# Performance work log

Measured on AMD Instinct MI355X. Metric: run time of the kernel, lower is better.

Reference implementation:

```python
import jax, jax.numpy as jnp
import numpy as np
from jax import lax

EPS = 1e-5

def _conv3x3(x, w, stride=1):
    # x: [B,C,H,W], w: [O,I,3,3]
    dn = lax.conv_dimension_numbers(x.shape, w.shape, ('NCHW', 'OIHW', 'NCHW'))
    return lax.conv_general_dilated(x, w, window_strides=(stride, stride),
                                    padding=((1, 1), (1, 1)), dimension_numbers=dn)

def _batchnorm(x, gamma, beta):
    # training-mode BN over (N,H,W) per channel
    mean = jnp.mean(x, axis=(0, 2, 3), keepdims=True)
    var = jnp.var(x, axis=(0, 2, 3), keepdims=True)
    inv = lax.rsqrt(var + EPS)
    return (x - mean) * inv * gamma[None, :, None, None] + beta[None, :, None, None]

def setup_inputs() -> dict:
    key = jax.random.key(0)
    ks = jax.random.split(key, 8)
    B, C, H, W, E = 16, 256, 64, 64, 512
    x = jax.random.normal(ks[0], (B, C, H, W), dtype=jnp.float32)
    embedding = jax.random.normal(ks[1], (B, E), dtype=jnp.float32)
    s_conv = 1.0 / np.sqrt(C * 9)
    conv1_w = jax.random.normal(ks[2], (C, C, 3, 3), dtype=jnp.float32) * s_conv
    conv2_w = jax.random.normal(ks[3], (C, C, 3, 3), dtype=jnp.float32) * s_conv
    s_g = 1.0 / np.sqrt(E)
    g1_w = jax.random.normal(ks[4], (E, C), dtype=jnp.float32) * s_g
    g1_b = jnp.zeros((C,), dtype=jnp.float32)
    g2_w = jax.random.normal(ks[5], (E, C), dtype=jnp.float32) * s_g
    g2_b = jnp.zeros((C,), dtype=jnp.float32)
    bn1_g = jnp.ones((C,), dtype=jnp.float32)
    bn1_b = jnp.zeros((C,), dtype=jnp.float32)
    bn2_g = jnp.ones((C,), dtype=jnp.float32)
    bn2_b = jnp.zeros((C,), dtype=jnp.float32)
    return {"x": x, "embedding": embedding, "conv1_w": conv1_w, "conv2_w": conv2_w,
            "g1_w": g1_w, "g1_b": g1_b, "g2_w": g2_w, "g2_b": g2_b,
            "bn1_g": bn1_g, "bn1_b": bn1_b, "bn2_g": bn2_g, "bn2_b": bn2_b}

def reference(x, embedding, conv1_w, conv2_w, g1_w, g1_b, g2_w, g2_b,
              bn1_g, bn1_b, bn2_g, bn2_b):
    identity = x
    # gate 1: per-sample per-channel gate values (softmax over channels)
    gate1 = jax.nn.softmax(embedding @ g1_w + g1_b, axis=-1)  # [B,C]
    out = _conv3x3(x, conv1_w, stride=1) * gate1[:, :, None, None]
    out = jax.nn.relu(_batchnorm(out, bn1_g, bn1_b))
    # gate 2
    gate2 = jax.nn.softmax(embedding @ g2_w + g2_b, axis=-1)  # [B,C]
    out = _conv3x3(out, conv2_w, stride=1) * gate2[:, :, None, None]
    out = _batchnorm(out, bn2_g, bn2_b)
    out = jax.nn.relu(out + identity)
    return (out, gate1, gate2)
```

## Files before the change

kernel.cpp:

```cpp
#include <hip/hip_runtime.h>

typedef __attribute__((ext_vector_type(8))) short short8;
typedef __attribute__((ext_vector_type(4))) float f32x4;

#define HP 66

__device__ __forceinline__ unsigned short f2bf(float f) {
  unsigned u = __builtin_bit_cast(unsigned, f);
  u += 0x7FFFu + ((u >> 16) & 1u);
  return (unsigned short)(u >> 16);
}
__device__ __forceinline__ float bf2f(unsigned short h) {
  return __builtin_bit_cast(float, ((unsigned)h) << 16);
}
__device__ __forceinline__ __attribute__((address_space(3))) void* to_as3(void* p) {
  return (__attribute__((address_space(3))) void*)(unsigned)(unsigned long long)p;
}
__device__ __forceinline__ const __attribute__((address_space(1))) void* to_as1(const void* p) {
  return (const __attribute__((address_space(1))) void*)(unsigned long long)p;
}

#define SB0() __builtin_amdgcn_sched_barrier(0)
#define BAR() do { SB0(); __builtin_amdgcn_s_barrier(); SB0(); } while (0)

__global__ void k_halo_zero(unsigned int* xp) {
  int p = blockIdx.x % 260;
  int b = blockIdx.x / 260;
  int h, w;
  if (p < 66)      { h = 0;  w = p; }
  else if (p < 132){ h = 65; w = p - 66; }
  else             { int q = p - 132; h = 1 + (q >> 1); w = (q & 1) * 65; }
  unsigned int* dst = xp + ((long)((b*HP + h)*HP + w) * 256) / 2;
  dst[threadIdx.x] = 0u;
  dst[threadIdx.x + 64] = 0u;
}

__global__ __launch_bounds__(256) void k_convert_x(const float* __restrict__ x,
                                                   unsigned short* __restrict__ xp) {
  __shared__ float tile[32][65];
  int blk = blockIdx.x;
  int ct = blk & 7, h = (blk >> 3) & 63, b = blk >> 9;
  int c0 = ct * 32;
  int t = threadIdx.x;
  int w = t & 63, cs = t >> 6;
#pragma unroll
  for (int i = 0; i < 8; ++i) {
    int c = cs + i * 4;
    tile[c][w] = x[(((b * 256) + c0 + c) * 64 + h) * 64 + w];
  }
  __syncthreads();
  int cl = (t & 15) * 2, w0 = t >> 4;
#pragma unroll
  for (int i = 0; i < 4; ++i) {
    int ww = w0 + i * 16;
    unsigned v = (unsigned)f2bf(tile[cl][ww]) | ((unsigned)f2bf(tile[cl + 1][ww]) << 16);
    *(unsigned*)(xp + ((long)((b*HP + h + 1)*HP + (ww + 1)) * 256 + c0 + cl)) = v;
  }
}

__global__ void k_pack_w(const float* __restrict__ w, unsigned short* __restrict__ wT) {
  int co = blockIdx.x;
  int t = threadIdx.x;
#pragma unroll
  for (int kk = 0; kk < 9; ++kk) {
    wT[co * 2304 + kk * 256 + t] = f2bf(w[(co * 256 + t) * 9 + kk]);
  }
}

__global__ __launch_bounds__(256) void k_gates(const float* __restrict__ emb,
                                               const float* __restrict__ gw,
                                               const float* __restrict__ gbias,
                                               float* __restrict__ gout) {
  __shared__ float ebuf[512];
  __shared__ float red[8];
  int b = blockIdx.x, t = threadIdx.x;
  ebuf[t] = emb[b * 512 + t];
  ebuf[t + 256] = emb[b * 512 + t + 256];
  __syncthreads();
  float acc = gbias[t];
  for (int k = 0; k < 512; ++k) acc += ebuf[k] * gw[k * 256 + t];
  float mx = acc;
  for (int off = 32; off >= 1; off >>= 1) mx = fmaxf(mx, __shfl_xor(mx, off));
  if ((t & 63) == 0) red[t >> 6] = mx;
  __syncthreads();
  mx = fmaxf(fmaxf(red[0], red[1]), fmaxf(red[2], red[3]));
  float e = expf(acc - mx);
  float sm = e;
  for (int off = 32; off >= 1; off >>= 1) sm += __shfl_xor(sm, off);
  if ((t & 63) == 0) red[4 + (t >> 6)] = sm;
  __syncthreads();
  sm = red[4] + red[5] + red[6] + red[7];
  gout[b * 256 + t] = e / sm;
}

__global__ __launch_bounds__(512, 2) void k_conv(
    const unsigned short* __restrict__ inp,
    const unsigned short* __restrict__ wT,
    const float* __restrict__ gate,
    unsigned short* __restrict__ yout,
    float* __restrict__ partials) {
  __shared__ short As[2][256][64];
  __shared__ short Bs[2][256][64];
  __shared__ float sbuf[2][256][2];

  const int t = threadIdx.x;
  const int lane = t & 63;
  const int wid = t >> 6;
  const int wm = wid >> 2;
  const int wn = wid & 3;
  const int lr = lane & 15;
  const int hi = lane >> 4;
  const int key = lr & 7;

  const int blk = blockIdx.x;
  const int b = blk >> 4;
  const int hh4 = (blk & 15) << 2;

  const int r0 = t >> 3;
  const int cdst = (t & 7) << 3;
  const int cg8 = (((t & 7) ^ ((t >> 3) & 7)) << 3);

  int aoff[4];
#pragma unroll
  for (int i = 0; i < 4; ++i)
    aoff[i] = (b * HP + hh4 + i) * HP + r0;

  auto stageA = [&](int buf, int half, int s) {
    int kk = s >> 2;
    int kh = (kk * 11) >> 5;
    int khw = kh * 66 + (kk - kh * 3);
    int ci = ((s & 3) << 6) + cg8;
    const unsigned short* g0 = inp + (long)(aoff[half * 2 + 0] + khw) * 256 + ci;
    const unsigned short* g1 = inp + (long)(aoff[half * 2 + 1] + khw) * 256 + ci;
    __builtin_amdgcn_global_load_lds(to_as1(g0), to_as3((void*)&As[buf][half * 128 + r0][cdst]), 16, 0, 0);
    __builtin_amdgcn_global_load_lds(to_as1(g1), to_as3((void*)&As[buf][half * 128 + 64 + r0][cdst]), 16, 0, 0);
  };
  auto stageB = [&](int buf, int half, int s) {
    int co0 = half * 128 + r0;
    const unsigned short* g0 = wT + (long)co0 * 2304 + s * 64 + cg8;
    const unsigned short* g1 = wT + (long)(co0 + 64) * 2304 + s * 64 + cg8;
    __builtin_amdgcn_global_load_lds(to_as1(g0), to_as3((void*)&Bs[buf][half * 128 + r0][cdst]), 16, 0, 0);
    __builtin_amdgcn_global_load_lds(to_as1(g1), to_as3((void*)&Bs[buf][half * 128 + 64 + r0][cdst]), 16, 0, 0);
  };

  f32x4 acc[8][4];
#pragma unroll
  for (int i = 0; i < 8; ++i)
#pragma unroll
    for (int j = 0; j < 4; ++j) acc[i][j] = (f32x4){0.f, 0.f, 0.f, 0.f};

  stageA(0, 0, 0); stageA(0, 1, 0); stageB(0, 0, 0); stageB(0, 1, 0);
  stageA(1, 0, 1); stageA(1, 1, 1); stageB(1, 0, 1);
  asm volatile("s_waitcnt vmcnt(6)" ::: "memory");
  BAR();

  short8 afrag[8][2], bfrag[4][2];

#define QUAD(q)                                                                     \
  do {                                                                              \
    __builtin_amdgcn_s_setprio(1);                                                  \
    _Pragma("unroll") for (int ks = 0; ks < 2; ++ks)                                \
      _Pragma("unroll") for (int mo = 0; mo < 2; ++mo)                              \
        _Pragma("unroll") for (int nf = 0; nf < 4; ++nf)                            \
          acc[2 * (q) + mo][nf] = __builtin_amdgcn_mfma_f32_16x16x32_bf16(          \
              afrag[2 * (q) + mo][ks], bfrag[nf][ks], acc[2 * (q) + mo][nf], 0, 0, 0); \
    __builtin_amdgcn_s_setprio(0);                                                  \
  } while (0)

  for (int kt = 0; kt < 36; ++kt) {
    const int cur = kt & 1;
#pragma unroll
    for (int nf = 0; nf < 4; ++nf)
#pragma unroll
      for (int ks = 0; ks < 2; ++ks)
        bfrag[nf][ks] = *(const short8*)&Bs[cur][wn * 64 + nf * 16 + lr][((ks * 4 + hi) ^ key) << 3];
#pragma unroll
    for (int mf = 0; mf < 4; ++mf)
#pragma unroll
      for (int ks = 0; ks < 2; ++ks)
        afrag[mf][ks] = *(const short8*)&As[cur][wm * 128 + mf * 16 + lr][((ks * 4 + hi) ^ key) << 3];
    if (kt + 1 < 36) stageB(cur ^ 1, 1, kt + 1);
    BAR();
    QUAD(0);
    BAR();
#pragma unroll
    for (int mf = 4; mf < 8; ++mf)
#pragma unroll
      for (int ks = 0; ks < 2; ++ks)
        afrag[mf][ks] = *(const short8*)&As[cur][wm * 128 + mf * 16 + lr][((ks * 4 + hi) ^ key) << 3];
    BAR();
    QUAD(1);
    asm volatile("s_waitcnt lgkmcnt(0)" ::: "memory");
    BAR();
    if (kt + 2 < 36) stageA(cur, 0, kt + 2);
    BAR();
    QUAD(2);
    BAR();
    if (kt + 2 < 36) { stageA(cur, 1, kt + 2); stageB(cur, 0, kt + 2); }
    BAR();
    QUAD(3);
    if (kt < 34) asm volatile("s_waitcnt vmcnt(6)" ::: "memory");
    else         asm volatile("s_waitcnt vmcnt(0)" ::: "memory");
    BAR();
  }
#undef QUAD

  float g[4];
#pragma unroll
  for (int nf = 0; nf < 4; ++nf) g[nf] = gate[(b << 8) + wn * 64 + nf * 16 + lr];

  float s[4] = {0, 0, 0, 0}, sq[4] = {0, 0, 0, 0};
  const int mrow0 = (blk << 8) + wm * 128 + (hi << 2);
  const int c0 = wn * 64 + lr;
#pragma unroll
  for (int mf = 0; mf < 8; ++mf)
#pragma unroll
    for (int r = 0; r < 4; ++r) {
      const int mm = mrow0 + mf * 16 + r;
#pragma unroll
      for (int nf = 0; nf < 4; ++nf) {
        float v = acc[mf][nf][r] * g[nf];
        yout[(long)mm * 256 + c0 + nf * 16] = f2bf(v);
        s[nf] += v;
        sq[nf] += v * v;
      }
    }
#pragma unroll
  for (int nf = 0; nf < 4; ++nf) {
    s[nf] += __shfl_xor(s[nf], 16);  s[nf] += __shfl_xor(s[nf], 32);
    sq[nf] += __shfl_xor(sq[nf], 16); sq[nf] += __shfl_xor(sq[nf], 32);
  }
  if (hi == 0) {
#pragma unroll
    for (int nf = 0; nf < 4; ++nf) {
      int c = wn * 64 + nf * 16 + lr;
      sbuf[wm][c][0] = s[nf];
      sbuf[wm][c][1] = sq[nf];
    }
  }
  __syncthreads();
  if (t < 256) {
    partials[((blk << 8) + t) * 2]     = sbuf[0][t][0] + sbuf[1][t][0];
    partials[((blk << 8) + t) * 2 + 1] = sbuf[0][t][1] + sbuf[1][t][1];
  }
}

__global__ __launch_bounds__(256) void k_bnfin(const float* __restrict__ partials,
                                               const float* __restrict__ gamma,
                                               const float* __restrict__ beta,
                                               float2* __restrict__ aff) {
  __shared__ float red[8];
  int c = blockIdx.x, t = threadIdx.x;
  float s = partials[(t * 256 + c) * 2];
  float sq = partials[(t * 256 + c) * 2 + 1];
  for (int off = 32; off >= 1; off >>= 1) { s += __shfl_xor(s, off); sq += __shfl_xor(sq, off); }
  if ((t & 63) == 0) { red[t >> 6] = s; red[4 + (t >> 6)] = sq; }
  __syncthreads();
  if (t == 0) {
    s = red[0] + red[1] + red[2] + red[3];
    sq = red[4] + red[5] + red[6] + red[7];
    float mean = s * (1.0f / 65536.0f);
    float var = fmaxf(sq * (1.0f / 65536.0f) - mean * mean, 0.0f);
    float inv = rsqrtf(var + 1e-5f);
    float ga = gamma[c] * inv;
    aff[c] = make_float2(ga, beta[c] - mean * ga);
  }
}

__global__ __launch_bounds__(256) void k_mid(const unsigned short* __restrict__ y1,
                                             const float2* __restrict__ aff,
                                             unsigned short* __restrict__ zp) {
  long idx = (long)blockIdx.x * 256 + threadIdx.x;
  int c0 = (int)(idx & 31) * 8;
  long pos = idx >> 5;
  int b = (int)(pos >> 12), hw = (int)(pos & 4095);
  int h = hw >> 6, w = hw & 63;
  uint4 v = *(const uint4*)(y1 + pos * 256 + c0);
  unsigned vv[4] = {v.x, v.y, v.z, v.w};
  unsigned outp[4];
#pragma unroll
  for (int j = 0; j < 4; ++j) {
    float2 aL = aff[c0 + 2 * j], aH = aff[c0 + 2 * j + 1];
    float lo = fmaxf(aL.x * bf2f((unsigned short)(vv[j] & 0xFFFF)) + aL.y, 0.f);
    float hiv = fmaxf(aH.x * bf2f((unsigned short)(vv[j] >> 16)) + aH.y, 0.f);
    outp[j] = (unsigned)f2bf(lo) | ((unsigned)f2bf(hiv) << 16);
  }
  unsigned short* dst = zp + (long)((b * HP + h + 1) * HP + w + 1) * 256 + c0;
  *(uint4*)dst = make_uint4(outp[0], outp[1], outp[2], outp[3]);
}

__global__ __launch_bounds__(256) void k_final(const unsigned short* __restrict__ y2,
                                               const float2* __restrict__ aff,
                                               const float* __restrict__ x,
                                               float* __restrict__ out) {
  __shared__ float tile[64][33];
  int blk = blockIdx.x;
  int ct = blk & 7, h = (blk >> 3) & 63, b = blk >> 9;
  int c0 = ct * 32;
  int t = threadIdx.x;
  int cl = (t & 15) * 2, w0 = t >> 4;
#pragma unroll
  for (int i = 0; i < 4; ++i) {
    int w = w0 + i * 16;
    unsigned v = *(const unsigned*)(y2 + (long)((b * 4096) + h * 64 + w) * 256 + c0 + cl);
    float2 aL = aff[c0 + cl], aH = aff[c0 + cl + 1];
    tile[w][cl] = aL.x * bf2f((unsigned short)(v & 0xFFFF)) + aL.y;
    tile[w][cl + 1] = aH.x * bf2f((unsigned short)(v >> 16)) + aH.y;
  }
  __syncthreads();
  int w = t & 63, csub = t >> 6;
#pragma unroll
  for (int j = 0; j < 8; ++j) {
    int c = c0 + csub * 8 + j;
    long o = ((long)(b * 256 + c) * 64 + h) * 64 + w;
    out[o] = fmaxf(tile[w][csub * 8 + j] + x[o], 0.f);
  }
}

extern "C" void kernel_launch(void* const* d_in, const int* in_sizes, int n_in,
                              void* d_out, int out_size, void* d_ws, size_t ws_size,
                              hipStream_t stream) {
  const float* x    = (const float*)d_in[0];
  const float* emb  = (const float*)d_in[1];
  const float* w1   = (const float*)d_in[2];
  const float* w2   = (const float*)d_in[3];
  const float* g1w  = (const float*)d_in[4];
  const float* g1b  = (const float*)d_in[5];
  const float* g2w  = (const float*)d_in[6];
  const float* g2b  = (const float*)d_in[7];
  const float* bn1g = (const float*)d_in[8];
  const float* bn1b = (const float*)d_in[9];
  const float* bn2g = (const float*)d_in[10];
  const float* bn2b = (const float*)d_in[11];

  float* out = (float*)d_out;
  float* gate1 = out + 16777216;
  float* gate2 = gate1 + 4096;

  char* ws = (char*)d_ws;
  const size_t OFF_XP  = 0;
  const size_t OFF_WT1 = 35684352;
  const size_t OFF_WT2 = OFF_WT1 + 1179648;
  const size_t OFF_Y   = OFF_WT2 + 1179648;
  const size_t OFF_PART = OFF_Y + 33554432;
  const size_t OFF_AFF1 = OFF_PART + 1048576;
  const size_t OFF_AFF2 = OFF_AFF1 + 2048;

  unsigned short* xp  = (unsigned short*)(ws + OFF_XP);
  unsigned short* wT1 = (unsigned short*)(ws + OFF_WT1);
  unsigned short* wT2 = (unsigned short*)(ws + OFF_WT2);
  unsigned short* y   = (unsigned short*)(ws + OFF_Y);
  float* part = (float*)(ws + OFF_PART);
  float2* aff1 = (float2*)(ws + OFF_AFF1);
  float2* aff2 = (float2*)(ws + OFF_AFF2);

  k_halo_zero<<<16 * 260, 64, 0, stream>>>((unsigned int*)xp);
  k_convert_x<<<8192, 256, 0, stream>>>(x, xp);
  k_pack_w<<<256, 256, 0, stream>>>(w1, wT1);
  k_pack_w<<<256, 256, 0, stream>>>(w2, wT2);
  k_gates<<<16, 256, 0, stream>>>(emb, g1w, g1b, gate1);
  k_gates<<<16, 256, 0, stream>>>(emb, g2w, g2b, gate2);

  k_conv<<<256, 512, 0, stream>>>(xp, wT1, gate1, y, part);
  k_bnfin<<<256, 256, 0, stream>>>(part, bn1g, bn1b, aff1);
  k_mid<<<8192, 256, 0, stream>>>(y, aff1, xp);

  k_conv<<<256, 512, 0, stream>>>(xp, wT2, gate2, y, part);
  k_bnfin<<<256, 256, 0, stream>>>(part, bn2g, bn2b, aff2);
  k_final<<<8192, 256, 0, stream>>>(y, aff2, x, out);
}
```

Measured before the change: 247.2 us.

## Merge weight-pack and gate launches, swizzle conv block order, reorder MFMA quadrants

Combines the two weight-pack kernels and the two gate kernels into single launches using blockIdx.y, removing two kernel launches. Remaps conv block indices so consecutive blocks spread across XCDs/batches, changing L2 locality of the input tiles. Restructures the MFMA inner loop into 4x2 quadrants so only half the B fragments load before the first compute phase, overlapping LDS reads with MFMA. Each change is small but they are independent ideas.

```diff
diff --git a/kernel.cpp b/kernel.cpp
--- a/kernel.cpp
+++ b/kernel.cpp
@@ -58,7 +58,10 @@
   }
 }
 
-__global__ void k_pack_w(const float* __restrict__ w, unsigned short* __restrict__ wT) {
+__global__ void k_pack_w(const float* __restrict__ w1, const float* __restrict__ w2,
+                         unsigned short* __restrict__ wT1, unsigned short* __restrict__ wT2) {
+  const float* w = blockIdx.y ? w2 : w1;
+  unsigned short* wT = blockIdx.y ? wT2 : wT1;
   int co = blockIdx.x;
   int t = threadIdx.x;
 #pragma unroll
@@ -68,9 +71,15 @@
 }
 
 __global__ __launch_bounds__(256) void k_gates(const float* __restrict__ emb,
-                                               const float* __restrict__ gw,
-                                               const float* __restrict__ gbias,
-                                               float* __restrict__ gout) {
+                                               const float* __restrict__ g1w,
+                                               const float* __restrict__ g1b,
+                                               const float* __restrict__ g2w,
+                                               const float* __restrict__ g2b,
+                                               float* __restrict__ gate1,
+                                               float* __restrict__ gate2) {
+  const float* gw = blockIdx.y ? g2w : g1w;
+  const float* gbias = blockIdx.y ? g2b : g1b;
+  float* gout = blockIdx.y ? gate2 : gate1;
   __shared__ float ebuf[512];
   __shared__ float red[8];
   int b = blockIdx.x, t = threadIdx.x;
@@ -112,7 +121,7 @@
   const int hi = lane >> 4;
   const int key = lr & 7;
 
-  const int blk = blockIdx.x;
+  const int blk = ((blockIdx.x & 7) << 5) + (blockIdx.x >> 3);
   const int b = blk >> 4;
   const int hh4 = (blk & 15) << 2;
 
@@ -156,21 +165,22 @@
 
   short8 afrag[8][2], bfrag[4][2];
 
-#define QUAD(q)                                                                     \
-  do {                                                                              \
-    __builtin_amdgcn_s_setprio(1);                                                  \
-    _Pragma("unroll") for (int ks = 0; ks < 2; ++ks)                                \
-      _Pragma("unroll") for (int mo = 0; mo < 2; ++mo)                              \
-        _Pragma("unroll") for (int nf = 0; nf < 4; ++nf)                            \
-          acc[2 * (q) + mo][nf] = __builtin_amdgcn_mfma_f32_16x16x32_bf16(          \
-              afrag[2 * (q) + mo][ks], bfrag[nf][ks], acc[2 * (q) + mo][nf], 0, 0, 0); \
-    __builtin_amdgcn_s_setprio(0);                                                  \
+#define QUAD2(mh, nh)                                                                \
+  do {                                                                               \
+    __builtin_amdgcn_s_setprio(1);                                                   \
+    _Pragma("unroll") for (int ks = 0; ks < 2; ++ks)                                 \
+      _Pragma("unroll") for (int mo = 0; mo < 4; ++mo)                               \
+        _Pragma("unroll") for (int no = 0; no < 2; ++no)                             \
+          acc[(mh) * 4 + mo][(nh) * 2 + no] = __builtin_amdgcn_mfma_f32_16x16x32_bf16( \
+              afrag[(mh) * 4 + mo][ks], bfrag[(nh) * 2 + no][ks],                    \
+              acc[(mh) * 4 + mo][(nh) * 2 + no], 0, 0, 0);                           \
+    __builtin_amdgcn_s_setprio(0);                                                   \
   } while (0)
 
   for (int kt = 0; kt < 36; ++kt) {
     const int cur = kt & 1;
 #pragma unroll
-    for (int nf = 0; nf < 4; ++nf)
+    for (int nf = 0; nf < 2; ++nf)
 #pragma unroll
       for (int ks = 0; ks < 2; ++ks)
         bfrag[nf][ks] = *(const short8*)&Bs[cur][wn * 64 + nf * 16 + lr][((ks * 4 + hi) ^ key) << 3];
@@ -181,29 +191,34 @@
         afrag[mf][ks] = *(const short8*)&As[cur][wm * 128 + mf * 16 + lr][((ks * 4 + hi) ^ key) << 3];
     if (kt + 1 < 36) stageB(cur ^ 1, 1, kt + 1);
     BAR();
-    QUAD(0);
-    BAR();
+    QUAD2(0, 0);
+    BAR();
+#pragma unroll
+    for (int nf = 2; nf < 4; ++nf)
+#pragma unroll
+      for (int ks = 0; ks < 2; ++ks)
+        bfrag[nf][ks] = *(const short8*)&Bs[cur][wn * 64 + nf * 16 + lr][((ks * 4 + hi) ^ key) << 3];
 #pragma unroll
     for (int mf = 4; mf < 8; ++mf)
 #pragma unroll
       for (int ks = 0; ks < 2; ++ks)
         afrag[mf][ks] = *(const short8*)&As[cur][wm * 128 + mf * 16 + lr][((ks * 4 + hi) ^ key) << 3];
     BAR();
-    QUAD(1);
+    QUAD2(1, 1);
     asm volatile("s_waitcnt lgkmcnt(0)" ::: "memory");
     BAR();
     if (kt + 2 < 36) stageA(cur, 0, kt + 2);
     BAR();
-    QUAD(2);
+    QUAD2(0, 1);
     BAR();
     if (kt + 2 < 36) { stageA(cur, 1, kt + 2); stageB(cur, 0, kt + 2); }
     BAR();
-    QUAD(3);
+    QUAD2(1, 0);
     if (kt < 34) asm volatile("s_waitcnt vmcnt(6)" ::: "memory");
     else         asm volatile("s_waitcnt vmcnt(0)" ::: "memory");
     BAR();
   }
-#undef QUAD
+#undef QUAD2
 
   float g[4];
 #pragma unroll
@@ -356,10 +371,8 @@
 
   k_halo_zero<<<16 * 260, 64, 0, stream>>>((unsigned int*)xp);
   k_convert_x<<<8192, 256, 0, stream>>>(x, xp);
-  k_pack_w<<<256, 256, 0, stream>>>(w1, wT1);
-  k_pack_w<<<256, 256, 0, stream>>>(w2, wT2);
-  k_gates<<<16, 256, 0, stream>>>(emb, g1w, g1b, gate1);
-  k_gates<<<16, 256, 0, stream>>>(emb, g2w, g2b, gate2);
+  k_pack_w<<<dim3(256, 2), 256, 0, stream>>>(w1, w2, wT1, wT2);
+  k_gates<<<dim3(16, 2), 256, 0, stream>>>(emb, g1w, g1b, g2w, g2b, gate1, gate2);
 
   k_conv<<<256, 512, 0, stream>>>(xp, wT1, gate1, y, part);
   k_bnfin<<<256, 256, 0, stream>>>(part, bn1g, bn1b, aff1);
```

Measured after the change: 230.3 us. 6.8% less time.
